# Kernel tuning notes

Hardware: AMD Instinct MI355X
Metric: run time of the kernel (lower is better)

## Reference

```python
import jax, jax.numpy as jnp
import numpy as np

BN_EPS = 1e-5
C = 128  # channels (hardcoded by feed_forward convs)


def _bn(v, gamma, beta, mean, var):
    # BatchNorm1d in inference form over channel axis of [B, C, N]
    scale = gamma / jnp.sqrt(var + BN_EPS)
    return (v - mean[:, None]) * scale[:, None] + beta[:, None]


def setup_inputs() -> dict:
    key = jax.random.key(0)
    ks = jax.random.split(key, 8)
    B, N = 8, 2048
    s = 0.05
    return {
        "x": jax.random.normal(ks[0], (B, N, C), jnp.float32),
        "Wq": jax.random.normal(ks[1], (C // 4, C), jnp.float32) * s,
        "Wk": jax.random.normal(ks[2], (C // 4, C), jnp.float32) * s,
        "Wv": jax.random.normal(ks[3], (C, C), jnp.float32) * s,
        "bv": jnp.zeros((C,), jnp.float32),
        "Wt": jax.random.normal(ks[4], (C, C), jnp.float32) * s,
        "bt": jnp.zeros((C,), jnp.float32),
        "g1": jnp.ones((C,), jnp.float32),
        "b1": jnp.zeros((C,), jnp.float32),
        "m1": jnp.zeros((C,), jnp.float32),
        "v1": jnp.ones((C,), jnp.float32),
        "W1": jax.random.normal(ks[5], (512, C), jnp.float32) * s,
        "bf1": jnp.zeros((512,), jnp.float32),
        "W2": jax.random.normal(ks[6], (C, 512), jnp.float32) * s,
        "bf2": jnp.zeros((C,), jnp.float32),
        "g2": jnp.ones((C,), jnp.float32),
        "b2": jnp.zeros((C,), jnp.float32),
        "m2": jnp.zeros((C,), jnp.float32),
        "v2": jnp.ones((C,), jnp.float32),
    }


def reference(x, Wq, Wk, Wv, bv, Wt, bt, g1, b1, m1, v1,
              W1, bf1, W2, bf2, g2, b2, m2, v2):
    # x: [B, N, C] -> work in [B, C, N] layout like the torch module
    xc = jnp.transpose(x, (0, 2, 1))                      # [B, C, N]
    # q_conv(x).permute -> [B, N, C/4]; k_conv -> [B, C/4, N]
    x_q = jnp.einsum('bnc,oc->bno', x, Wq)                # [B, N, C/4]
    x_k = jnp.einsum('bnc,oc->bon', x, Wk)                # [B, C/4, N]
    x_v = jnp.einsum('bnc,oc->bon', x, Wv) + bv[:, None]  # [B, C, N]

    energy = jnp.einsum('bnd,bdm->bnm', x_q, x_k)         # [B, N, N]
    scale = jnp.sqrt(jnp.asarray(C, x.dtype))             # sqrt(x_v.shape[-2])
    attention = jax.nn.softmax(energy / scale, axis=-1)   # [B, N, N]
    x_r = jnp.einsum('bcn,bnm->bcm', x_v, attention)      # [B, C, N]

    t = jnp.einsum('oc,bcn->bon', Wt, xc - x_r) + bt[:, None]
    x_r2 = jax.nn.relu(_bn(t, g1, b1, m1, v1))
    h = xc + x_r2                                         # [B, C, N]

    residual = h
    f = jax.nn.relu(jnp.einsum('oc,bcn->bon', W1, h) + bf1[:, None])
    f = jnp.einsum('of,bfn->bon', W2, f) + bf2[:, None]
    out = _bn(residual + f, g2, b2, m2, v2)               # [B, C, N]
    return jnp.transpose(out, (0, 2, 1))                  # [B, N, C]
```

## Files before the change

### kernel.cpp

```cpp
#include <hip/hip_runtime.h>
#include <hip/hip_bf16.h>

#define BDIM 256
#define NPTS (8 * 2048)
#define CC 128
#define DD 32
#define FF 512
#define NN 2048
#define SCALE 0.08838834764831845f

typedef float f32x4 __attribute__((ext_vector_type(4)));
typedef short s16x8 __attribute__((ext_vector_type(8)));
typedef unsigned short ushort_t;

__device__ __forceinline__ ushort_t bf16r(float x) {
    __hip_bfloat16 h = __float2bfloat16(x);
    return *reinterpret_cast<ushort_t*>(&h);
}
__device__ __forceinline__ float bf16tof(ushort_t u) {
    unsigned v = ((unsigned)u) << 16;
    return *reinterpret_cast<float*>(&v);
}
__device__ __forceinline__ unsigned pack2(float a, float b) {
    return ((unsigned)bf16r(b) << 16) | (unsigned)bf16r(a);
}

__global__ void k_cvt_all(const float* __restrict__ W1, const float* __restrict__ W2,
                          const float* __restrict__ Wq, const float* __restrict__ Wk,
                          const float* __restrict__ Wv, const float* __restrict__ Wt,
                          ushort_t* __restrict__ dst) {
    int i = blockIdx.x * BDIM + threadIdx.x;
    const float* src; int off;
    if (i < 16384)      { src = W1; off = 0; }
    else if (i < 32768) { src = W2; off = 16384; }
    else if (i < 33792) { src = Wq; off = 32768; }
    else if (i < 34816) { src = Wk; off = 33792; }
    else if (i < 38912) { src = Wv; off = 34816; }
    else                { src = Wt; off = 38912; }
    float4 v = ((const float4*)src)[i - off];
    *(uint2*)(dst + (long)i * 4) = make_uint2(pack2(v.x, v.y), pack2(v.z, v.w));
}

__global__ __launch_bounds__(256) void k_proj(
        const float* __restrict__ x, const ushort_t* __restrict__ Wb,
        const float* __restrict__ bv,
        ushort_t* __restrict__ qg, ushort_t* __restrict__ kg,
        ushort_t* __restrict__ vTg) {
    __shared__ ushort_t xs[32][136];
    __shared__ ushort_t qks[32][72];
    __shared__ ushort_t vs[32][136];
    long base = (long)blockIdx.x * 32;
    int b = (int)(base >> 11);
    int n0 = (int)(base & (NN - 1));
    int t = threadIdx.x, w = t >> 6, l = t & 63, a = l & 15, g = l >> 4;
    {
        const float4* xg4 = (const float4*)(x + base * CC);
        #pragma unroll
        for (int rep = 0; rep < 4; ++rep) {
            int i = rep * BDIM + t;
            float4 v4 = xg4[i];
            int p = i >> 5, c4 = (i & 31) * 4;
            *(uint2*)&xs[p][c4] = make_uint2(pack2(v4.x, v4.y), pack2(v4.z, v4.w));
        }
    }
    s16x8 bF[3][4];
    #pragma unroll
    for (int ct = 0; ct < 3; ++ct) {
        int ctg = w * 3 + ct;
        #pragma unroll
        for (int ki = 0; ki < 4; ++ki)
            bF[ct][ki] = *(const s16x8*)(Wb + ((long)(ctg * 16 + a)) * CC + ki * 32 + g * 8);
    }
    __syncthreads();
    #pragma unroll
    for (int rt = 0; rt < 2; ++rt) {
        s16x8 aF[4];
        #pragma unroll
        for (int ki = 0; ki < 4; ++ki)
            aF[ki] = *(const s16x8*)&xs[rt * 16 + a][ki * 32 + g * 8];
        #pragma unroll
        for (int ct = 0; ct < 3; ++ct) {
            f32x4 acc = (f32x4){0.f, 0.f, 0.f, 0.f};
            #pragma unroll
            for (int ki = 0; ki < 4; ++ki)
                acc = __builtin_amdgcn_mfma_f32_16x16x32_bf16(aF[ki], bF[ct][ki], acc, 0, 0, 0);
            int ctg = w * 3 + ct;
            int oc = ctg * 16 + a;
            float bias = (oc >= 64) ? bv[oc - 64] : 0.f;
            #pragma unroll
            for (int r = 0; r < 4; ++r) {
                int p = rt * 16 + g * 4 + r;
                float val = acc[r] + bias;
                if (oc < 64) qks[p][oc] = bf16r(val);
                else         vs[p][oc - 64] = bf16r(val);
            }
        }
    }
    __syncthreads();
    {
        int p = t >> 3, c = (t & 7) * 4;
        *(uint2*)(qg + (base + p) * DD + c) = *(const uint2*)&qks[p][c];
        *(uint2*)(kg + (base + p) * DD + c) = *(const uint2*)&qks[p][32 + c];
    }
    #pragma unroll
    for (int rep = 0; rep < 2; ++rep) {
        int i = rep * BDIM + t;
        int c = i & 127, nch = i >> 7;
        int p0 = nch * 8;
        uint4 r;
        r.x = (unsigned)vs[p0+0][c] | ((unsigned)vs[p0+1][c] << 16);
        r.y = (unsigned)vs[p0+2][c] | ((unsigned)vs[p0+3][c] << 16);
        r.z = (unsigned)vs[p0+4][c] | ((unsigned)vs[p0+5][c] << 16);
        r.w = (unsigned)vs[p0+6][c] | ((unsigned)vs[p0+7][c] << 16);
        *(uint4*)(vTg + ((long)(b * CC + c)) * NN + n0 + p0) = r;
    }
}

__global__ __launch_bounds__(256) void k_rowstats(
        const ushort_t* __restrict__ qg, const ushort_t* __restrict__ kg,
        float* __restrict__ rowinv) {
    __shared__ float ps[4][64];
    int b = blockIdx.x >> 5;
    int nt = (blockIdx.x & 31) * 64;
    int t = threadIdx.x, w = t >> 6, l = t & 63, a = l & 15, g = l >> 4;
    s16x8 qA[4];
    #pragma unroll
    for (int s = 0; s < 4; ++s)
        qA[s] = *(const s16x8*)(qg + ((long)(b * NN + nt + s*16 + a)) * DD + g*8);
    float sm[16];
    #pragma unroll
    for (int i = 0; i < 16; ++i) sm[i] = 0.f;
    s16x8 kB = *(const s16x8*)(kg + ((long)(b * NN + w * 16 + a)) * DD + g*8);
    for (int it = 0; it < 32; ++it) {
        s16x8 kBn;
        if (it < 31)
            kBn = *(const s16x8*)(kg + ((long)(b * NN + ((it+1)*4 + w)*16 + a)) * DD + g*8);
        #pragma unroll
        for (int s = 0; s < 4; ++s) {
            f32x4 D = (f32x4){0.f, 0.f, 0.f, 0.f};
            D = __builtin_amdgcn_mfma_f32_16x16x32_bf16(qA[s], kB, D, 0, 0, 0);
            #pragma unroll
            for (int r = 0; r < 4; ++r)
                sm[s * 4 + r] += __expf(D[r] * SCALE);
        }
        kB = kBn;
    }
    #pragma unroll
    for (int off = 1; off < 16; off <<= 1)
        #pragma unroll
        for (int ix = 0; ix < 16; ++ix)
            sm[ix] += __shfl_xor(sm[ix], off, 64);
    if (a == 0) {
        #pragma unroll
        for (int s = 0; s < 4; ++s)
            #pragma unroll
            for (int r = 0; r < 4; ++r)
                ps[w][s * 16 + g * 4 + r] = sm[s * 4 + r];
    }
    __syncthreads();
    if (t < 64) {
        float S = ps[0][t] + ps[1][t] + ps[2][t] + ps[3][t];
        rowinv[(long)b * NN + nt + t] = 1.f / S;
    }
}

__global__ __launch_bounds__(512) void k_pv(
        const ushort_t* __restrict__ qg, const ushort_t* __restrict__ kg,
        const ushort_t* __restrict__ vTg, const float* __restrict__ rowinv,
        float* __restrict__ xr) {
    __shared__ ushort_t qs[2][64][40];
    __shared__ ushort_t ks[32][40];
    __shared__ ushort_t vTs[2][128][72];
    __shared__ ushort_t pT[32][72];
    __shared__ float rin_s[2][64];
    int b = blockIdx.x >> 6;
    int m0 = (blockIdx.x & 63) * 32;
    int t = threadIdx.x, w = t >> 6, l = t & 63, a = l & 15, g = l >> 4;
    int nsub = w & 3, msub = w >> 2;
    const ushort_t* vTb = vTg + (long)b * CC * NN;
    if (t < 128) {
        int r = t >> 2, o = (t & 3) * 8;
        *(s16x8*)&ks[r][o] = *(const s16x8*)(kg + ((long)(b * NN + m0 + r)) * DD + o);
    }
    int qr = t >> 2, qo = (t & 3) * 8;
    int c0 = t >> 3, vo0 = (t & 7) * 8;
    int c1 = (512 + t) >> 3, vo1 = (t & 7) * 8;
    uint4 qreg = make_uint4(0, 0, 0, 0), vreg0, vreg1;
    float rinreg = 0.f;
    if (t < 256) qreg = *(const uint4*)(qg + ((long)(b * NN + qr)) * DD + qo);
    vreg0 = *(const uint4*)(vTb + (long)c0 * NN + vo0);
    vreg1 = *(const uint4*)(vTb + (long)c1 * NN + vo1);
    if (t < 64) rinreg = rowinv[(long)b * NN + t];
    if (t < 256) *(uint4*)&qs[0][qr][qo] = qreg;
    *(uint4*)&vTs[0][c0][vo0] = vreg0;
    *(uint4*)&vTs[0][c1][vo1] = vreg1;
    if (t < 64) rin_s[0][t] = rinreg;

    f32x4 acc[2];
    acc[0] = (f32x4){0.f, 0.f, 0.f, 0.f};
    acc[1] = (f32x4){0.f, 0.f, 0.f, 0.f};
    int cur = 0;
    for (int it = 0; it < 32; ++it) {
        __syncthreads();
        int ntn = (it + 1) * 64;
        if (it < 31) {
            if (t < 256) qreg = *(const uint4*)(qg + ((long)(b * NN + ntn + qr)) * DD + qo);
            vreg0 = *(const uint4*)(vTb + (long)c0 * NN + ntn + vo0);
            vreg1 = *(const uint4*)(vTb + (long)c1 * NN + ntn + vo1);
            if (t < 64) rinreg = rowinv[(long)b * NN + ntn + t];
        }
        s16x8 qf = *(const s16x8*)&qs[cur][nsub * 16 + a][g * 8];
        s16x8 kf = *(const s16x8*)&ks[msub * 16 + a][g * 8];
        f32x4 e = (f32x4){0.f, 0.f, 0.f, 0.f};
        e = __builtin_amdgcn_mfma_f32_16x16x32_bf16(qf, kf, e, 0, 0, 0);
        float p[4];
        #pragma unroll
        for (int r = 0; r < 4; ++r)
            p[r] = __expf(e[r] * SCALE) * rin_s[cur][nsub * 16 + g * 4 + r];
        *(uint2*)&pT[msub * 16 + a][nsub * 16 + g * 4] =
            make_uint2(pack2(p[0], p[1]), pack2(p[2], p[3]));
        __syncthreads();
        #pragma unroll
        for (int k2 = 0; k2 < 2; ++k2) {
            s16x8 A0 = *(const s16x8*)&pT[a][k2 * 32 + g * 8];
            s16x8 A1 = *(const s16x8*)&pT[16 + a][k2 * 32 + g * 8];
            s16x8 Bf = *(const s16x8*)&vTs[cur][w * 16 + a][k2 * 32 + g * 8];
            acc[0] = __builtin_amdgcn_mfma_f32_16x16x32_bf16(A0, Bf, acc[0], 0, 0, 0);
            acc[1] = __builtin_amdgcn_mfma_f32_16x16x32_bf16(A1, Bf, acc[1], 0, 0, 0);
        }
        if (it < 31) {
            if (t < 256) *(uint4*)&qs[cur ^ 1][qr][qo] = qreg;
            *(uint4*)&vTs[cur ^ 1][c0][vo0] = vreg0;
            *(uint4*)&vTs[cur ^ 1][c1][vo1] = vreg1;
            if (t < 64) rin_s[cur ^ 1][t] = rinreg;
        }
        cur ^= 1;
    }
    #pragma unroll
    for (int ms = 0; ms < 2; ++ms)
        #pragma unroll
        for (int r = 0; r < 4; ++r) {
            int m = m0 + ms * 16 + g * 4 + r;
            xr[((long)b * NN + m) * CC + w * 16 + a] = acc[ms][r];
        }
}

__global__ __launch_bounds__(256) void k_tproj(
        const float* __restrict__ x, const float* __restrict__ xr,
        const ushort_t* __restrict__ Wtb, const float* __restrict__ bt,
        const float* __restrict__ g1, const float* __restrict__ b1,
        const float* __restrict__ m1, const float* __restrict__ v1,
        ushort_t* __restrict__ hb) {
    __shared__ ushort_t ds[32][136];
    __shared__ ushort_t xb[32][136];
    __shared__ ushort_t wt[128][136];
    long base = (long)blockIdx.x * 32;
    int t = threadIdx.x, l = t & 63, wid = t >> 6;
    int ph = wid & 1, fh = wid >> 1;
    int lr = l & 15, lg = l >> 4;
    {
        const float4* xg4 = (const float4*)(x + base * CC);
        const float4* rg4 = (const float4*)(xr + base * CC);
        #pragma unroll
        for (int rep = 0; rep < 4; ++rep) {
            int i = rep * BDIM + t;
            float4 xv = xg4[i], rv = rg4[i];
            int p = i >> 5, c4 = (i & 31) * 4;
            *(uint2*)&ds[p][c4] = make_uint2(pack2(xv.x - rv.x, xv.y - rv.y),
                                             pack2(xv.z - rv.z, xv.w - rv.w));
            *(uint2*)&xb[p][c4] = make_uint2(pack2(xv.x, xv.y), pack2(xv.z, xv.w));
        }
    }
    {
        #pragma unroll
        for (int rep = 0; rep < 8; ++rep) {
            int i = rep * BDIM + t;
            int r = i >> 4, cc0 = (i & 15) * 8;
            *(uint4*)&wt[r][cc0] = *(const uint4*)(Wtb + (long)r * CC + cc0);
        }
    }
    __syncthreads();
    s16x8 aF[4];
    #pragma unroll
    for (int ki = 0; ki < 4; ++ki)
        aF[ki] = *(const s16x8*)&ds[ph * 16 + lr][ki * 32 + lg * 8];
    #pragma unroll
    for (int oi = 0; oi < 4; ++oi) {
        int ot = fh * 4 + oi;
        f32x4 acc = (f32x4){0.f, 0.f, 0.f, 0.f};
        #pragma unroll
        for (int ki = 0; ki < 4; ++ki) {
            s16x8 bF = *(const s16x8*)&wt[ot * 16 + lr][ki * 32 + lg * 8];
            acc = __builtin_amdgcn_mfma_f32_16x16x32_bf16(aF[ki], bF, acc, 0, 0, 0);
        }
        int o = ot * 16 + lr;
        float sc = g1[o] * rsqrtf(v1[o] + 1e-5f);
        float mm = m1[o], bb = b1[o], bo = bt[o];
        #pragma unroll
        for (int r = 0; r < 4; ++r) {
            int p = ph * 16 + lg * 4 + r;
            float tv = ((acc[r] + bo) - mm) * sc + bb;
            tv = fmaxf(tv, 0.f);
            hb[(base + p) * CC + o] = bf16r(bf16tof(xb[p][o]) + tv);
        }
    }
}

__global__ __launch_bounds__(256) void k_ff(
        const ushort_t* __restrict__ hb, const ushort_t* __restrict__ W1b,
        const ushort_t* __restrict__ W2b,
        const float* __restrict__ bf1, const float* __restrict__ bf2,
        const float* __restrict__ g2, const float* __restrict__ b2,
        const float* __restrict__ m2, const float* __restrict__ v2,
        float* __restrict__ out) {
    __shared__ ushort_t hs[32][136];
    __shared__ ushort_t w1s[2][64][128];
    __shared__ ushort_t w2s[2][128][64];
    __shared__ ushort_t fss[32][72];
    long pbase = (long)blockIdx.x * 32;
    int t = threadIdx.x;
    int l = t & 63, wid = t >> 6;
    int ph = wid & 1, fh = wid >> 1;
    int lr = l & 15, lg = l >> 4;
    for (int i = t; i < 512; i += BDIM) {
        int r = i >> 4, c0 = (i & 15) * 8;
        *(uint4*)&hs[r][c0] = *(const uint4*)(hb + (pbase + r) * CC + c0);
    }
    #pragma unroll
    for (int rep = 0; rep < 4; ++rep) {
        int i = rep * BDIM + t;
        int r = i >> 4, c0 = (i & 15) * 8;
        *(uint4*)&w1s[0][r][c0 ^ ((r & 7) * 8)] = *(const uint4*)(W1b + (long)r * CC + c0);
    }
    #pragma unroll
    for (int rep = 0; rep < 4; ++rep) {
        int i = rep * BDIM + t;
        int r = i >> 3, c0 = (i & 7) * 8;
        *(uint4*)&w2s[0][r][c0 ^ ((r & 7) * 8)] = *(const uint4*)(W2b + (long)r * FF + c0);
    }
    __syncthreads();
    s16x8 hA[4];
    #pragma unroll
    for (int ki = 0; ki < 4; ++ki)
        hA[ki] = *(const s16x8*)&hs[ph * 16 + lr][ki * 32 + lg * 8];
    f32x4 acc2[4];
    #pragma unroll
    for (int i = 0; i < 4; ++i) acc2[i] = (f32x4){0.f, 0.f, 0.f, 0.f};

    int cur = 0;
    uint4 wrg0, wrg1, wrg2, wrg3, wrg4, wrg5, wrg6, wrg7;
    for (int fc = 0; fc < 8; ++fc) {
        if (fc) __syncthreads();
        int f0 = fc * 64;
        if (fc < 7) {
            int f0n = f0 + 64;
            int r1 = t >> 4, c1 = (t & 15) * 8;
            int r2 = t >> 3, c2 = (t & 7) * 8;
            wrg0 = *(const uint4*)(W1b + (long)(f0n + r1) * CC + c1);
            wrg1 = *(const uint4*)(W1b + (long)(f0n + 16 + r1) * CC + c1);
            wrg2 = *(const uint4*)(W1b + (long)(f0n + 32 + r1) * CC + c1);
            wrg3 = *(const uint4*)(W1b + (long)(f0n + 48 + r1) * CC + c1);
            wrg4 = *(const uint4*)(W2b + (long)r2 * FF + f0n + c2);
            wrg5 = *(const uint4*)(W2b + (long)(32 + r2) * FF + f0n + c2);
            wrg6 = *(const uint4*)(W2b + (long)(64 + r2) * FF + f0n + c2);
            wrg7 = *(const uint4*)(W2b + (long)(96 + r2) * FF + f0n + c2);
        }
        #pragma unroll
        for (int fi = 0; fi < 2; ++fi) {
            int ft = fh * 2 + fi;
            int row = ft * 16 + lr;
            f32x4 a1 = (f32x4){0.f, 0.f, 0.f, 0.f};
            #pragma unroll
            for (int ki = 0; ki < 4; ++ki) {
                int col = ki * 32 + lg * 8;
                s16x8 bfr = *(const s16x8*)&w1s[cur][row][col ^ ((row & 7) * 8)];
                a1 = __builtin_amdgcn_mfma_f32_16x16x32_bf16(hA[ki], bfr, a1, 0, 0, 0);
            }
            float bias = bf1[f0 + ft * 16 + lr];
            #pragma unroll
            for (int r = 0; r < 4; ++r) {
                float vv = fmaxf(a1[r] + bias, 0.f);
                fss[ph * 16 + lg * 4 + r][ft * 16 + lr] = bf16r(vv);
            }
        }
        __syncthreads();
        #pragma unroll
        for (int k2 = 0; k2 < 2; ++k2) {
            s16x8 afr = *(const s16x8*)&fss[ph * 16 + lr][k2 * 32 + lg * 8];
            #pragma unroll
            for (int oi = 0; oi < 4; ++oi) {
                int ot = fh * 4 + oi;
                int row = ot * 16 + lr;
                int col = k2 * 32 + lg * 8;
                s16x8 bfr = *(const s16x8*)&w2s[cur][row][col ^ ((row & 7) * 8)];
                acc2[oi] = __builtin_amdgcn_mfma_f32_16x16x32_bf16(afr, bfr, acc2[oi], 0, 0, 0);
            }
        }
        if (fc < 7) {
            int nb = cur ^ 1;
            int r1 = t >> 4, c1 = (t & 15) * 8;
            int r2 = t >> 3, c2 = (t & 7) * 8;
            *(uint4*)&w1s[nb][r1][c1 ^ ((r1 & 7) * 8)] = wrg0;
            *(uint4*)&w1s[nb][16 + r1][c1 ^ ((r1 & 7) * 8)] = wrg1;
            *(uint4*)&w1s[nb][32 + r1][c1 ^ ((r1 & 7) * 8)] = wrg2;
            *(uint4*)&w1s[nb][48 + r1][c1 ^ ((r1 & 7) * 8)] = wrg3;
            *(uint4*)&w2s[nb][r2][c2 ^ ((r2 & 7) * 8)] = wrg4;
            *(uint4*)&w2s[nb][32 + r2][c2 ^ (((32 + r2) & 7) * 8)] = wrg5;
            *(uint4*)&w2s[nb][64 + r2][c2 ^ (((64 + r2) & 7) * 8)] = wrg6;
            *(uint4*)&w2s[nb][96 + r2][c2 ^ (((96 + r2) & 7) * 8)] = wrg7;
            cur = nb;
        }
    }
    #pragma unroll
    for (int oi = 0; oi < 4; ++oi) {
        int o = (fh * 4 + oi) * 16 + lr;
        float sc = g2[o] * rsqrtf(v2[o] + 1e-5f);
        float mm = m2[o], bb = b2[o], bias2 = bf2[o];
        #pragma unroll
        for (int r = 0; r < 4; ++r) {
            int p = ph * 16 + lg * 4 + r;
            float val = bf16tof(hs[p][o]) + acc2[oi][r] + bias2;
            out[(pbase + p) * CC + o] = (val - mm) * sc + bb;
        }
    }
}

extern "C" void kernel_launch(void* const* d_in, const int* in_sizes, int n_in,
                              void* d_out, int out_size, void* d_ws, size_t ws_size,
                              hipStream_t stream) {
    const float* x   = (const float*)d_in[0];
    const float* Wq  = (const float*)d_in[1];
    const float* Wk  = (const float*)d_in[2];
    const float* Wv  = (const float*)d_in[3];
    const float* bv  = (const float*)d_in[4];
    const float* Wt  = (const float*)d_in[5];
    const float* bt  = (const float*)d_in[6];
    const float* g1  = (const float*)d_in[7];
    const float* b1  = (const float*)d_in[8];
    const float* m1  = (const float*)d_in[9];
    const float* v1  = (const float*)d_in[10];
    const float* W1  = (const float*)d_in[11];
    const float* bf1 = (const float*)d_in[12];
    const float* W2  = (const float*)d_in[13];
    const float* bf2 = (const float*)d_in[14];
    const float* g2  = (const float*)d_in[15];
    const float* b2  = (const float*)d_in[16];
    const float* m2  = (const float*)d_in[17];
    const float* v2  = (const float*)d_in[18];
    float* out = (float*)d_out;

    float* ws  = (float*)d_ws;
    float* xr  = ws;
    float* rin = xr + (long)NPTS * CC;
    ushort_t* qg   = (ushort_t*)(rin + NPTS);
    ushort_t* kg   = qg + (long)NPTS * DD;
    ushort_t* vTg  = kg + (long)NPTS * DD;
    ushort_t* hbuf = vTg + (long)NPTS * CC;
    ushort_t* W1b  = hbuf + (long)NPTS * CC;
    ushort_t* W2b  = W1b + FF * CC;
    ushort_t* Wb   = W2b + FF * CC;
    ushort_t* Wtb  = Wb + 192 * CC;

    k_cvt_all<<<168, BDIM, 0, stream>>>(W1, W2, Wq, Wk, Wv, Wt, W1b);
    k_proj<<<NPTS / 32, BDIM, 0, stream>>>(x, Wb, bv, qg, kg, vTg);
    k_rowstats<<<8 * (NN / 64), BDIM, 0, stream>>>(qg, kg, rin);
    k_pv<<<8 * (NN / 32), 512, 0, stream>>>(qg, kg, vTg, rin, xr);
    k_tproj<<<NPTS / 32, BDIM, 0, stream>>>(x, xr, Wtb, bt, g1, b1, m1, v1, hbuf);
    k_ff<<<NPTS / 32, BDIM, 0, stream>>>(hbuf, W1b, W2b, bf1, bf2, g2, b2, m2, v2, out);
}
```

Baseline: 81.70 us.

## Fuse trans-projection, BN1, ReLU and residual into the PV attention kernel epilogue

Removes the separate k_tproj kernel and the fp32 xr workspace round-trip. The PV kernel now stages x for its 32-point tile in shared memory, forms x - x_r in bf16 in LDS, and runs the Wt MFMA projection with BN, ReLU and the residual add in its epilogue, writing hb directly. This saves one launch and about 8 MB of global write plus read traffic. In exchange it adds LDS to the PV kernel, which may lower occupancy. Wt fragments are now read straight from global memory instead of being staged in LDS.

```diff
diff --git a/kernel.cpp b/kernel.cpp
--- a/kernel.cpp
+++ b/kernel.cpp
@@ -167,12 +167,18 @@
 __global__ __launch_bounds__(512) void k_pv(
         const ushort_t* __restrict__ qg, const ushort_t* __restrict__ kg,
         const ushort_t* __restrict__ vTg, const float* __restrict__ rowinv,
-        float* __restrict__ xr) {
+        const float* __restrict__ x, const ushort_t* __restrict__ Wtb,
+        const float* __restrict__ bt,
+        const float* __restrict__ g1, const float* __restrict__ b1,
+        const float* __restrict__ m1, const float* __restrict__ v1,
+        ushort_t* __restrict__ hb) {
     __shared__ ushort_t qs[2][64][40];
     __shared__ ushort_t ks[32][40];
     __shared__ ushort_t vTs[2][128][72];
     __shared__ ushort_t pT[32][72];
     __shared__ float rin_s[2][64];
+    __shared__ ushort_t xb[32][136];
+    __shared__ ushort_t ds[32][136];
     int b = blockIdx.x >> 6;
     int m0 = (blockIdx.x & 63) * 32;
     int t = threadIdx.x, w = t >> 6, l = t & 63, a = l & 15, g = l >> 4;
@@ -236,72 +242,52 @@
         }
         cur ^= 1;
     }
+    long pbase = (long)b * NN + m0;
+    {
+        const float4* xg4 = (const float4*)(x + pbase * CC);
+        #pragma unroll
+        for (int rep = 0; rep < 2; ++rep) {
+            int i = rep * 512 + t;
+            float4 xv = xg4[i];
+            int p = i >> 5, c4 = (i & 31) * 4;
+            *(uint2*)&xb[p][c4] = make_uint2(pack2(xv.x, xv.y), pack2(xv.z, xv.w));
+        }
+    }
+    __syncthreads();
     #pragma unroll
     for (int ms = 0; ms < 2; ++ms)
         #pragma unroll
         for (int r = 0; r < 4; ++r) {
-            int m = m0 + ms * 16 + g * 4 + r;
-            xr[((long)b * NN + m) * CC + w * 16 + a] = acc[ms][r];
-        }
-}
-
-__global__ __launch_bounds__(256) void k_tproj(
-        const float* __restrict__ x, const float* __restrict__ xr,
-        const ushort_t* __restrict__ Wtb, const float* __restrict__ bt,
-        const float* __restrict__ g1, const float* __restrict__ b1,
-        const float* __restrict__ m1, const float* __restrict__ v1,
-        ushort_t* __restrict__ hb) {
-    __shared__ ushort_t ds[32][136];
-    __shared__ ushort_t xb[32][136];
-    __shared__ ushort_t wt[128][136];
-    long base = (long)blockIdx.x * 32;
-    int t = threadIdx.x, l = t & 63, wid = t >> 6;
-    int ph = wid & 1, fh = wid >> 1;
-    int lr = l & 15, lg = l >> 4;
+            int ml = ms * 16 + g * 4 + r;
+            int c = w * 16 + a;
+            ds[ml][c] = bf16r(bf16tof(xb[ml][c]) - acc[ms][r]);
+        }
+    __syncthreads();
     {
-        const float4* xg4 = (const float4*)(x + base * CC);
-        const float4* rg4 = (const float4*)(xr + base * CC);
-        #pragma unroll
-        for (int rep = 0; rep < 4; ++rep) {
-            int i = rep * BDIM + t;
-            float4 xv = xg4[i], rv = rg4[i];
-            int p = i >> 5, c4 = (i & 31) * 4;
-            *(uint2*)&ds[p][c4] = make_uint2(pack2(xv.x - rv.x, xv.y - rv.y),
-                                             pack2(xv.z - rv.z, xv.w - rv.w));
-            *(uint2*)&xb[p][c4] = make_uint2(pack2(xv.x, xv.y), pack2(xv.z, xv.w));
-        }
-    }
-    {
-        #pragma unroll
-        for (int rep = 0; rep < 8; ++rep) {
-            int i = rep * BDIM + t;
-            int r = i >> 4, cc0 = (i & 15) * 8;
-            *(uint4*)&wt[r][cc0] = *(const uint4*)(Wtb + (long)r * CC + cc0);
-        }
-    }
-    __syncthreads();
-    s16x8 aF[4];
-    #pragma unroll
-    for (int ki = 0; ki < 4; ++ki)
-        aF[ki] = *(const s16x8*)&ds[ph * 16 + lr][ki * 32 + lg * 8];
-    #pragma unroll
-    for (int oi = 0; oi < 4; ++oi) {
-        int ot = fh * 4 + oi;
-        f32x4 acc = (f32x4){0.f, 0.f, 0.f, 0.f};
-        #pragma unroll
-        for (int ki = 0; ki < 4; ++ki) {
-            s16x8 bF = *(const s16x8*)&wt[ot * 16 + lr][ki * 32 + lg * 8];
-            acc = __builtin_amdgcn_mfma_f32_16x16x32_bf16(aF[ki], bF, acc, 0, 0, 0);
-        }
-        int o = ot * 16 + lr;
-        float sc = g1[o] * rsqrtf(v1[o] + 1e-5f);
-        float mm = m1[o], bb = b1[o], bo = bt[o];
-        #pragma unroll
-        for (int r = 0; r < 4; ++r) {
-            int p = ph * 16 + lg * 4 + r;
-            float tv = ((acc[r] + bo) - mm) * sc + bb;
-            tv = fmaxf(tv, 0.f);
-            hb[(base + p) * CC + o] = bf16r(bf16tof(xb[p][o]) + tv);
+        int ph = w & 1, fh = w >> 1;
+        s16x8 aF[4];
+        #pragma unroll
+        for (int ki = 0; ki < 4; ++ki)
+            aF[ki] = *(const s16x8*)&ds[ph * 16 + a][ki * 32 + g * 8];
+        #pragma unroll
+        for (int oi = 0; oi < 2; ++oi) {
+            int ot = fh * 2 + oi;
+            f32x4 ac = (f32x4){0.f, 0.f, 0.f, 0.f};
+            #pragma unroll
+            for (int ki = 0; ki < 4; ++ki) {
+                s16x8 bF = *(const s16x8*)(Wtb + ((long)(ot * 16 + a)) * CC + ki * 32 + g * 8);
+                ac = __builtin_amdgcn_mfma_f32_16x16x32_bf16(aF[ki], bF, ac, 0, 0, 0);
+            }
+            int o = ot * 16 + a;
+            float sc = g1[o] * rsqrtf(v1[o] + 1e-5f);
+            float mm = m1[o], bb = b1[o], bo = bt[o];
+            #pragma unroll
+            for (int r = 0; r < 4; ++r) {
+                int p = ph * 16 + g * 4 + r;
+                float tv = ((ac[r] + bo) - mm) * sc + bb;
+                tv = fmaxf(tv, 0.f);
+                hb[(pbase + p) * CC + o] = bf16r(bf16tof(xb[p][o]) + tv);
+            }
         }
     }
 }
@@ -450,8 +436,7 @@
     float* out = (float*)d_out;
 
     float* ws  = (float*)d_ws;
-    float* xr  = ws;
-    float* rin = xr + (long)NPTS * CC;
+    float* rin = ws;
     ushort_t* qg   = (ushort_t*)(rin + NPTS);
     ushort_t* kg   = qg + (long)NPTS * DD;
     ushort_t* vTg  = kg + (long)NPTS * DD;
@@ -464,7 +449,7 @@
     k_cvt_all<<<168, BDIM, 0, stream>>>(W1, W2, Wq, Wk, Wv, Wt, W1b);
     k_proj<<<NPTS / 32, BDIM, 0, stream>>>(x, Wb, bv, qg, kg, vTg);
     k_rowstats<<<8 * (NN / 64), BDIM, 0, stream>>>(qg, kg, rin);
-    k_pv<<<8 * (NN / 32), 512, 0, stream>>>(qg, kg, vTg, rin, xr);
-    k_tproj<<<NPTS / 32, BDIM, 0, stream>>>(x, xr, Wtb, bt, g1, b1, m1, v1, hbuf);
+    k_pv<<<8 * (NN / 32), 512, 0, stream>>>(qg, kg, vTg, rin,
+                                            x, Wtb, bt, g1, b1, m1, v1, hbuf);
     k_ff<<<NPTS / 32, BDIM, 0, stream>>>(hbuf, W1b, W2b, bf1, bf2, g2, b2, m2, v2, out);
 }
```

Measured after the change: 80.62 us. About the same (-1.3%).
